# Kernel tuning notes

Hardware: AMD Instinct MI355X
Metric: run time of the kernel (lower is better)

## Reference

```python
import jax, jax.numpy as jnp
import numpy as np

N_GRAPHS = 100
BN_EPS = 1e-5
L = 4


def batch_norm(x, gamma, beta):
    # torch BatchNorm1d in training mode: biased batch statistics over the node dim
    mu = jnp.mean(x, axis=0)
    var = jnp.var(x, axis=0)
    return gamma * (x - mu) * jax.lax.rsqrt(var + BN_EPS) + beta


def setup_inputs() -> dict:
    key = jax.random.key(0)
    ks = jax.random.split(key, 24)
    N, E, IN, H, C = 50000, 600000, 128, 128, 10
    s = 0.05
    inp = {
        "h": jax.random.normal(ks[0], (N, IN), jnp.float32),
        "snorm_n": jax.random.uniform(ks[1], (N, 1), jnp.float32),
        "edge_src": jax.random.randint(ks[2], (E,), 0, N, jnp.int32),
        "edge_dst": jax.random.randint(ks[3], (E,), 0, N, jnp.int32),
        "graph_ids": jnp.sort(jax.random.randint(ks[4], (N,), 0, N_GRAPHS, jnp.int32)),
        # embedding_h
        "emb_W": jax.random.normal(ks[5], (IN, H), jnp.float32) * s,
        "emb_b": jnp.zeros((H,), jnp.float32),
        # per-layer GIN params, stacked over L layers
        "eps": jnp.zeros((L,), jnp.float32),
        "W1": jax.random.normal(ks[6], (L, H, H), jnp.float32) * s,
        "b1": jnp.zeros((L, H), jnp.float32),
        "g1": jnp.ones((L, H), jnp.float32),   # MLP internal BN gamma
        "be1": jnp.zeros((L, H), jnp.float32),  # MLP internal BN beta
        "W2": jax.random.normal(ks[7], (L, H, H), jnp.float32) * s,
        "b2": jnp.zeros((L, H), jnp.float32),
        "ga": jnp.ones((L, H), jnp.float32),    # ApplyNodeFunc BN gamma
        "ba": jnp.zeros((L, H), jnp.float32),
        "gl": jnp.ones((L, H), jnp.float32),    # GINLayer node BN gamma
        "bl": jnp.zeros((L, H), jnp.float32),
        # linears_prediction (L+1 of them)
        "pred_W": jax.random.normal(ks[8], (L + 1, H, C), jnp.float32) * s,
        "pred_b": jnp.zeros((L + 1, C), jnp.float32),
    }
    return inp


def reference(h, snorm_n, edge_src, edge_dst, graph_ids, emb_W, emb_b, eps,
              W1, b1, g1, be1, W2, b2, ga, ba, gl, bl, pred_W, pred_b):
    N = h.shape[0]
    h = h @ emb_W + emb_b  # embedding_h
    hidden_rep = [h]
    for i in range(L):
        h_in = h
        # sum-aggregate neighbor features (irregular gather + scatter-add)
        neigh = jax.ops.segment_sum(h[edge_src], edge_dst, num_segments=N)
        z = (1.0 + eps[i]) * h + neigh
        # ApplyNodeFunc: MLP (lin->BN->relu->lin) then BN then relu
        z = jax.nn.relu(batch_norm(z @ W1[i] + b1[i], g1[i], be1[i]))
        z = z @ W2[i] + b2[i]
        z = jax.nn.relu(batch_norm(z, ga[i], ba[i]))
        z = z * snorm_n                      # graph_norm
        z = batch_norm(z, gl[i], bl[i])      # batch_norm
        z = jax.nn.relu(z)
        h = h_in + z                         # residual (dropout p=0)
        hidden_rep.append(h)
    score = jnp.zeros((N_GRAPHS, pred_W.shape[-1]), h.dtype)
    for i, hr in enumerate(hidden_rep):
        pooled = jax.ops.segment_sum(hr, graph_ids, num_segments=N_GRAPHS)
        score = score + pooled @ pred_W[i] + pred_b[i]
    return score
```

## Files before the change

kernel.cpp:

```cpp
#include <hip/hip_runtime.h>

#define HD __device__ __forceinline__

static constexpr int H = 128;
static constexpr int G = 100;
static constexpr int L = 4;
static constexpr int C = 10;
static constexpr int DEGCAP = 64;

typedef __attribute__((ext_vector_type(8))) short short8;
typedef __attribute__((ext_vector_type(4))) float f32x4;

HD float bf2f(unsigned int u16) {
    return __uint_as_float(u16 << 16);
}
HD unsigned int f2bf(float f) {
    unsigned int u = __float_as_uint(f);
    u += 0x7fffu + ((u >> 16) & 1u);
    return u >> 16;
}

__global__ __launch_bounds__(256) void wprep_kernel(const float* __restrict__ embW,
                                                    const float* __restrict__ W1,
                                                    const float* __restrict__ W2,
                                                    unsigned short* __restrict__ WT) {
    int mat = blockIdx.y;
    const float* src = (mat == 0) ? embW
                     : (mat <= L) ? W1 + (size_t)(mat - 1) * H * H
                                  : W2 + (size_t)(mat - 1 - L) * H * H;
    int t = blockIdx.x * 256 + threadIdx.x;
    int col = t >> 7, k = t & 127;
    WT[(size_t)mat * H * H + col * H + k] = (unsigned short)f2bf(src[(size_t)k * H + col]);
}

__global__ void fill_kernel(const int* __restrict__ src, const int* __restrict__ dst, int E,
                            int* __restrict__ cnt, int* __restrict__ esrc) {
    int e = blockIdx.x * blockDim.x + threadIdx.x;
    if (e < E) {
        int d = dst[e];
        int pos = atomicAdd(&cnt[d], 1) & (DEGCAP - 1);
        esrc[(size_t)d * DEGCAP + pos] = src[e];
    }
}

__global__ __launch_bounds__(256, 4) void aggemm_kernel(
    const unsigned short* __restrict__ Hb, const int* __restrict__ cnt,
    const int* __restrict__ esrc, const float* __restrict__ eps, int layer,
    const unsigned short* __restrict__ WT, const float* __restrict__ bias,
    unsigned short* __restrict__ outB, int N,
    float* __restrict__ sum_out, float* __restrict__ sq_out) {
    __shared__ unsigned short As[64 * 136];
    int tid = threadIdx.x;
    int w = tid >> 6, lane = tid & 63, q = lane >> 4, m = lane & 15;
    int row0 = blockIdx.x * 64;
    int colbase = w * 32;

    short8 bfrag[2][4];
#pragma unroll
    for (int nt = 0; nt < 2; ++nt) {
        const unsigned short* wc = WT + (size_t)(colbase + nt * 16 + m) * H;
#pragma unroll
        for (int kk = 0; kk < 4; ++kk)
            bfrag[nt][kk] = *(const short8*)&wc[kk * 32 + q * 8];
    }

    const unsigned int* H2 = (const unsigned int*)Hb;
    float e1 = 1.0f + eps[layer];
    for (int i = 0; i < 16; ++i) {
        int r = w * 16 + i;
        int node = row0 + r;
        unsigned int out = 0;
        if (node < N) {
            unsigned int hv = H2[(size_t)node * 64 + lane];
            float ax[8], ay[8];
            ax[0] = e1 * bf2f(hv & 0xffffu);
            ay[0] = e1 * bf2f(hv >> 16);
#pragma unroll
            for (int u = 1; u < 8; ++u) { ax[u] = 0.f; ay[u] = 0.f; }
            int deg = min(cnt[node], DEGCAP);
            const int* ep = esrc + (size_t)node * DEGCAP;
            int j = 0;
            for (; j + 7 < deg; j += 8) {
                unsigned int v[8];
#pragma unroll
                for (int u = 0; u < 8; ++u) v[u] = H2[(size_t)ep[j + u] * 64 + lane];
#pragma unroll
                for (int u = 0; u < 8; ++u) {
                    ax[u] += bf2f(v[u] & 0xffffu);
                    ay[u] += bf2f(v[u] >> 16);
                }
            }
            for (; j + 1 < deg; j += 2) {
                unsigned int v0 = H2[(size_t)ep[j] * 64 + lane];
                unsigned int v1 = H2[(size_t)ep[j + 1] * 64 + lane];
                ax[0] += bf2f(v0 & 0xffffu); ay[0] += bf2f(v0 >> 16);
                ax[1] += bf2f(v1 & 0xffffu); ay[1] += bf2f(v1 >> 16);
            }
            if (j < deg) {
                unsigned int v0 = H2[(size_t)ep[j] * 64 + lane];
                ax[0] += bf2f(v0 & 0xffffu); ay[0] += bf2f(v0 >> 16);
            }
            float axs = ((ax[0] + ax[1]) + (ax[2] + ax[3])) + ((ax[4] + ax[5]) + (ax[6] + ax[7]));
            float ays = ((ay[0] + ay[1]) + (ay[2] + ay[3])) + ((ay[4] + ay[5]) + (ay[6] + ay[7]));
            out = f2bf(axs) | (f2bf(ays) << 16);
        }
        *(unsigned int*)&As[r * 136 + lane * 2] = out;
    }
    __syncthreads();

    f32x4 acc[4][2];
#pragma unroll
    for (int mt = 0; mt < 4; ++mt)
#pragma unroll
        for (int nt = 0; nt < 2; ++nt) acc[mt][nt] = (f32x4){0.f, 0.f, 0.f, 0.f};
#pragma unroll
    for (int kk = 0; kk < 4; ++kk) {
        short8 af[4];
#pragma unroll
        for (int mt = 0; mt < 4; ++mt)
            af[mt] = *(const short8*)&As[(mt * 16 + m) * 136 + kk * 32 + q * 8];
#pragma unroll
        for (int mt = 0; mt < 4; ++mt)
#pragma unroll
            for (int nt = 0; nt < 2; ++nt)
                acc[mt][nt] = __builtin_amdgcn_mfma_f32_16x16x32_bf16(
                    af[mt], bfrag[nt][kk], acc[mt][nt], 0, 0, 0);
    }

    float bs2[2] = {bias[colbase + m], bias[colbase + 16 + m]};
    float s[2] = {0.f, 0.f}, qq[2] = {0.f, 0.f};
#pragma unroll
    for (int mt = 0; mt < 4; ++mt)
#pragma unroll
        for (int nt = 0; nt < 2; ++nt) {
            int gcol = colbase + nt * 16 + m;
#pragma unroll
            for (int rg = 0; rg < 4; ++rg) {
                int grow = row0 + mt * 16 + q * 4 + rg;
                float v = acc[mt][nt][rg] + bs2[nt];
                if (grow < N) {
                    outB[(size_t)grow * H + gcol] = (unsigned short)f2bf(v);
                    s[nt] += v;
                    qq[nt] += v * v;
                }
            }
        }
#pragma unroll
    for (int nt = 0; nt < 2; ++nt) {
        float sv = s[nt], qv = qq[nt];
        sv += __shfl_xor(sv, 16); sv += __shfl_xor(sv, 32);
        qv += __shfl_xor(qv, 16); qv += __shfl_xor(qv, 32);
        if (q == 0) {
            atomicAdd(&sum_out[colbase + nt * 16 + m], sv);
            atomicAdd(&sq_out[colbase + nt * 16 + m], qv);
        }
    }
}

template <bool ABF16, bool TRANS, bool STATS, bool POOLF>
__global__ __launch_bounds__(256, 4) void mgemm_kernel(
    const float* __restrict__ Af, const unsigned short* __restrict__ Ab,
    const unsigned short* __restrict__ WT, const float* __restrict__ bias,
    const float* __restrict__ sum_in, const float* __restrict__ sq_in,
    const float* __restrict__ gam, const float* __restrict__ bet, float invN,
    unsigned short* __restrict__ outB,
    int N, float* __restrict__ sum_out, float* __restrict__ sq_out,
    const int* __restrict__ gids, float* __restrict__ pool) {
    __shared__ unsigned short As[64 * 136];
    __shared__ float cas[H], ccs[H];
    int tid = threadIdx.x;
    int w = tid >> 6, lane = tid & 63, q = lane >> 4, m = lane & 15;
    int row0 = blockIdx.x * 64;
    int colbase = w * 32;

    short8 bfrag[2][4];
#pragma unroll
    for (int nt = 0; nt < 2; ++nt) {
        const unsigned short* wc = WT + (size_t)(colbase + nt * 16 + m) * H;
#pragma unroll
        for (int kk = 0; kk < 4; ++kk)
            bfrag[nt][kk] = *(const short8*)&wc[kk * 32 + q * 8];
    }

    if (TRANS) {
        if (tid < H) {
            float mu = sum_in[tid] * invN;
            float var = sq_in[tid] * invN - mu * mu;
            float inv = rsqrtf(var + 1e-5f);
            float a = gam[tid] * inv;
            cas[tid] = a;
            ccs[tid] = bet[tid] - mu * a;
        }
        __syncthreads();
    }

    {
        int cc = tid & 15, rg = tid >> 4;
        int c0 = cc * 8;
        float a8[8], b8[8];
        if (TRANS) {
#pragma unroll
            for (int j = 0; j < 8; ++j) { a8[j] = cas[c0 + j]; b8[j] = ccs[c0 + j]; }
        }
#pragma unroll
        for (int rr = 0; rr < 4; ++rr) {
            int r = rg * 4 + rr;
            int gr = row0 + r;
            uint4 o = {0u, 0u, 0u, 0u};
            if (ABF16 && !TRANS) {
                if (gr < N) o = *(const uint4*)&Ab[(size_t)gr * H + c0];
            } else {
                float v[8] = {0.f, 0.f, 0.f, 0.f, 0.f, 0.f, 0.f, 0.f};
                if (gr < N) {
                    if (ABF16) {
                        uint4 x = *(const uint4*)&Ab[(size_t)gr * H + c0];
                        v[0] = bf2f(x.x & 0xffffu); v[1] = bf2f(x.x >> 16);
                        v[2] = bf2f(x.y & 0xffffu); v[3] = bf2f(x.y >> 16);
                        v[4] = bf2f(x.z & 0xffffu); v[5] = bf2f(x.z >> 16);
                        v[6] = bf2f(x.w & 0xffffu); v[7] = bf2f(x.w >> 16);
                    } else {
                        float4 x0 = *(const float4*)&Af[(size_t)gr * H + c0];
                        float4 x1 = *(const float4*)&Af[(size_t)gr * H + c0 + 4];
                        v[0] = x0.x; v[1] = x0.y; v[2] = x0.z; v[3] = x0.w;
                        v[4] = x1.x; v[5] = x1.y; v[6] = x1.z; v[7] = x1.w;
                    }
                }
                if (TRANS) {
#pragma unroll
                    for (int j = 0; j < 8; ++j) v[j] = fmaxf(a8[j] * v[j] + b8[j], 0.f);
                }
                o.x = f2bf(v[0]) | (f2bf(v[1]) << 16);
                o.y = f2bf(v[2]) | (f2bf(v[3]) << 16);
                o.z = f2bf(v[4]) | (f2bf(v[5]) << 16);
                o.w = f2bf(v[6]) | (f2bf(v[7]) << 16);
            }
            *(uint4*)&As[r * 136 + c0] = o;
        }
    }
    __syncthreads();

    f32x4 acc[4][2];
#pragma unroll
    for (int mt = 0; mt < 4; ++mt)
#pragma unroll
        for (int nt = 0; nt < 2; ++nt) acc[mt][nt] = (f32x4){0.f, 0.f, 0.f, 0.f};
#pragma unroll
    for (int kk = 0; kk < 4; ++kk) {
        short8 af[4];
#pragma unroll
        for (int mt = 0; mt < 4; ++mt)
            af[mt] = *(const short8*)&As[(mt * 16 + m) * 136 + kk * 32 + q * 8];
#pragma unroll
        for (int mt = 0; mt < 4; ++mt)
#pragma unroll
            for (int nt = 0; nt < 2; ++nt)
                acc[mt][nt] = __builtin_amdgcn_mfma_f32_16x16x32_bf16(
                    af[mt], bfrag[nt][kk], acc[mt][nt], 0, 0, 0);
    }

    float bs2[2] = {bias[colbase + m], bias[colbase + 16 + m]};
    float s[2] = {0.f, 0.f}, qq[2] = {0.f, 0.f};
#pragma unroll
    for (int mt = 0; mt < 4; ++mt)
#pragma unroll
        for (int nt = 0; nt < 2; ++nt) {
            int gcol = colbase + nt * 16 + m;
#pragma unroll
            for (int rg = 0; rg < 4; ++rg) {
                int grow = row0 + mt * 16 + q * 4 + rg;
                float v = acc[mt][nt][rg] + bs2[nt];
                if (grow < N) {
                    outB[(size_t)grow * H + gcol] = (unsigned short)f2bf(v);
                    if (STATS || POOLF) {
                        s[nt] += v;
                        if (STATS) qq[nt] += v * v;
                    }
                }
            }
        }

    if (STATS) {
#pragma unroll
        for (int nt = 0; nt < 2; ++nt) {
            float sv = s[nt], qv = qq[nt];
            sv += __shfl_xor(sv, 16); sv += __shfl_xor(sv, 32);
            qv += __shfl_xor(qv, 16); qv += __shfl_xor(qv, 32);
            if (q == 0) {
                atomicAdd(&sum_out[colbase + nt * 16 + m], sv);
                atomicAdd(&sq_out[colbase + nt * 16 + m], qv);
            }
        }
    }

    if (POOLF) {
        int last = min(row0 + 63, N - 1);
        bool uni = (gids[row0] == gids[last]);
        if (uni) {
            int g = gids[row0];
#pragma unroll
            for (int nt = 0; nt < 2; ++nt) {
                float sv = s[nt];
                sv += __shfl_xor(sv, 16); sv += __shfl_xor(sv, 32);
                if (q == 0) atomicAdd(&pool[g * H + colbase + nt * 16 + m], sv);
            }
        } else {
#pragma unroll
            for (int mt = 0; mt < 4; ++mt)
#pragma unroll
                for (int nt = 0; nt < 2; ++nt)
#pragma unroll
                    for (int rg = 0; rg < 4; ++rg) {
                        int grow = row0 + mt * 16 + q * 4 + rg;
                        if (grow < N) {
                            float v = acc[mt][nt][rg] + bs2[nt];
                            atomicAdd(&pool[gids[grow] * H + colbase + nt * 16 + m], v);
                        }
                    }
        }
    }
}

__global__ __launch_bounds__(256) void statsv_kernel(const unsigned short* __restrict__ UB,
                                                     const float* __restrict__ snorm,
                                                     const float* __restrict__ sum2, const float* __restrict__ sq2,
                                                     const float* __restrict__ ga, const float* __restrict__ ba,
                                                     float invN, int N,
                                                     float* __restrict__ sum3, float* __restrict__ sq3) {
    __shared__ float cas[H], ccs[H];
    int t = threadIdx.x;
    if (t < H) {
        float m = sum2[t] * invN;
        float var = sq2[t] * invN - m * m;
        float inv = rsqrtf(var + 1e-5f);
        float a = ga[t] * inv;
        cas[t] = a;
        ccs[t] = ba[t] - m * a;
    }
    __syncthreads();
    int col2 = t & 63, part = t >> 6;
    int c0 = col2 * 2, c1 = c0 + 1;
    float a0 = cas[c0], b0 = ccs[c0], a1 = cas[c1], b1 = ccs[c1];
    float s0 = 0.f, q0 = 0.f, s1 = 0.f, q1 = 0.f;
    const unsigned int* U2 = (const unsigned int*)UB;
    for (int r = blockIdx.x * 4 + part; r < N; r += gridDim.x * 4) {
        float sn = snorm[r];
        unsigned int v = U2[(size_t)r * 64 + col2];
        float v0 = fmaxf(a0 * bf2f(v & 0xffffu) + b0, 0.f) * sn;
        float v1 = fmaxf(a1 * bf2f(v >> 16) + b1, 0.f) * sn;
        s0 += v0; q0 += v0 * v0;
        s1 += v1; q1 += v1 * v1;
    }
    __shared__ float S[4][H], Q[4][H];
    S[part][c0] = s0; S[part][c1] = s1;
    Q[part][c0] = q0; Q[part][c1] = q1;
    __syncthreads();
    if (t < H) {
        atomicAdd(&sum3[t], S[0][t] + S[1][t] + S[2][t] + S[3][t]);
        atomicAdd(&sq3[t], Q[0][t] + Q[1][t] + Q[2][t] + Q[3][t]);
    }
}

__global__ __launch_bounds__(256) void tail_kernel(unsigned short* __restrict__ Hb,
                                                   const unsigned short* __restrict__ UB,
                                                   const float* __restrict__ snorm,
                                                   const float* __restrict__ sum2, const float* __restrict__ sq2,
                                                   const float* __restrict__ ga, const float* __restrict__ ba,
                                                   const float* __restrict__ sum3, const float* __restrict__ sq3,
                                                   const float* __restrict__ gl, const float* __restrict__ bl,
                                                   float invN, const int* __restrict__ gids,
                                                   float* __restrict__ pool, int N) {
    __shared__ float ca2[H], cc2[H], ca3[H], cc3[H];
    __shared__ float PS[8][H];
    int t = threadIdx.x;
    if (t < H) {
        float m2 = sum2[t] * invN, v2 = sq2[t] * invN - m2 * m2;
        float i2 = rsqrtf(v2 + 1e-5f), a2 = ga[t] * i2;
        ca2[t] = a2; cc2[t] = ba[t] - m2 * a2;
        float m3 = sum3[t] * invN, v3 = sq3[t] * invN - m3 * m3;
        float i3 = rsqrtf(v3 + 1e-5f), a3 = gl[t] * i3;
        ca3[t] = a3; cc3[t] = bl[t] - m3 * a3;
    }
    __syncthreads();
    int row0 = blockIdx.x * 32;
    int col4 = t & 31, rowg = t >> 5;
    int c0 = col4 * 4;
    float A2[4], B2[4], A3[4], B3[4];
#pragma unroll
    for (int j = 0; j < 4; ++j) {
        A2[j] = ca2[c0 + j]; B2[j] = cc2[c0 + j];
        A3[j] = ca3[c0 + j]; B3[j] = cc3[c0 + j];
    }
    bool uni = (gids[row0] == gids[min(row0 + 31, N - 1)]);
    float p[4] = {0.f, 0.f, 0.f, 0.f};
    const uint2* U4 = (const uint2*)UB;
    uint2* H4 = (uint2*)Hb;
#pragma unroll
    for (int rr = 0; rr < 4; ++rr) {
        int r = row0 + rowg * 4 + rr;
        if (r < N) {
            float sn = snorm[r];
            uint2 uv = U4[(size_t)r * 32 + col4];
            uint2 hv = H4[(size_t)r * 32 + col4];
            float u[4] = {bf2f(uv.x & 0xffffu), bf2f(uv.x >> 16), bf2f(uv.y & 0xffffu), bf2f(uv.y >> 16)};
            float h[4] = {bf2f(hv.x & 0xffffu), bf2f(hv.x >> 16), bf2f(hv.y & 0xffffu), bf2f(hv.y >> 16)};
#pragma unroll
            for (int j = 0; j < 4; ++j) {
                float v = fmaxf(A2[j] * u[j] + B2[j], 0.f) * sn;
                h[j] += fmaxf(A3[j] * v + B3[j], 0.f);
            }
            uint2 hb;
            hb.x = f2bf(h[0]) | (f2bf(h[1]) << 16);
            hb.y = f2bf(h[2]) | (f2bf(h[3]) << 16);
            H4[(size_t)r * 32 + col4] = hb;
            if (uni) {
                p[0] += h[0]; p[1] += h[1]; p[2] += h[2]; p[3] += h[3];
            } else {
                int g = gids[r];
#pragma unroll
                for (int j = 0; j < 4; ++j) atomicAdd(&pool[g * H + c0 + j], h[j]);
            }
        }
    }
    if (uni) {
#pragma unroll
        for (int j = 0; j < 4; ++j) PS[rowg][c0 + j] = p[j];
        __syncthreads();
        if (t < H) {
            float s = PS[0][t] + PS[1][t] + PS[2][t] + PS[3][t] +
                      PS[4][t] + PS[5][t] + PS[6][t] + PS[7][t];
            atomicAdd(&pool[gids[row0] * H + t], s);
        }
    }
}

__global__ void final_kernel(const float* __restrict__ pool, const float* __restrict__ pw,
                             const float* __restrict__ pb, float* __restrict__ out) {
    int g = blockIdx.x, t = threadIdx.x;
    __shared__ float p[H];
    float acc = 0.f;
    for (int i = 0; i <= L; ++i) {
        p[t] = pool[(size_t)(i * G + g) * H + t];
        __syncthreads();
        if (t < C) {
            float s = 0.f;
            for (int f = 0; f < H; ++f) s += p[f] * pw[(size_t)(i * H + f) * C + t];
            acc += s + pb[i * C + t];
        }
        __syncthreads();
    }
    if (t < C) out[g * C + t] = acc;
}

extern "C" void kernel_launch(void* const* d_in, const int* in_sizes, int n_in,
                              void* d_out, int out_size, void* d_ws, size_t ws_size,
                              hipStream_t stream) {
    const float* h_in  = (const float*)d_in[0];
    const float* snorm = (const float*)d_in[1];
    const int* esrc_in = (const int*)d_in[2];
    const int* edst_in = (const int*)d_in[3];
    const int* gids    = (const int*)d_in[4];
    const float* embW = (const float*)d_in[5];
    const float* embB = (const float*)d_in[6];
    const float* eps  = (const float*)d_in[7];
    const float* W1   = (const float*)d_in[8];
    const float* b1   = (const float*)d_in[9];
    const float* g1   = (const float*)d_in[10];
    const float* be1  = (const float*)d_in[11];
    const float* W2   = (const float*)d_in[12];
    const float* b2   = (const float*)d_in[13];
    const float* ga   = (const float*)d_in[14];
    const float* ba   = (const float*)d_in[15];
    const float* gl   = (const float*)d_in[16];
    const float* bl   = (const float*)d_in[17];
    const float* predW = (const float*)d_in[18];
    const float* predB = (const float*)d_in[19];

    const int N = in_sizes[0] / H;
    const int E = in_sizes[2];
    const float invN = 1.0f / (float)N;

    float* ws = (float*)d_ws;
    float* POOL = ws;
    float* STATS = POOL + (size_t)(L + 1) * G * H;
    int* CNT = (int*)(STATS + (size_t)L * 6 * H);
    unsigned short* WT = (unsigned short*)(CNT + N);
    int* ESRC = (int*)(WT + (size_t)9 * H * H);
    unsigned short* Hb = (unsigned short*)(ESRC + (size_t)N * DEGCAP);
    unsigned short* TB = Hb + (size_t)N * H;
    unsigned short* UB = TB + (size_t)N * H;

    size_t zbytes = ((size_t)(L + 1) * G * H + (size_t)L * 6 * H + N) * 4;
    hipMemsetAsync(POOL, 0, zbytes, stream);

    wprep_kernel<<<dim3(64, 9), 256, 0, stream>>>(embW, W1, W2, WT);
    fill_kernel<<<(E + 255) / 256, 256, 0, stream>>>(esrc_in, edst_in, E, CNT, ESRC);

    int gblocks = (N + 63) / 64;
    mgemm_kernel<false, false, false, true><<<gblocks, 256, 0, stream>>>(
        h_in, nullptr, WT, embB, nullptr, nullptr, nullptr, nullptr, invN,
        Hb, N, nullptr, nullptr, gids, POOL);

    for (int i = 0; i < L; ++i) {
        float* S1 = STATS + (size_t)i * 6 * H;
        float* Q1 = S1 + H;
        float* S2 = Q1 + H;
        float* Q2 = S2 + H;
        float* S3 = Q2 + H;
        float* Q3 = S3 + H;
        aggemm_kernel<<<gblocks, 256, 0, stream>>>(
            Hb, CNT, ESRC, eps, i, WT + (size_t)(1 + i) * H * H, b1 + (size_t)i * H,
            TB, N, S1, Q1);
        mgemm_kernel<true, true, true, false><<<gblocks, 256, 0, stream>>>(
            nullptr, TB, WT + (size_t)(1 + L + i) * H * H, b2 + (size_t)i * H,
            S1, Q1, g1 + (size_t)i * H, be1 + (size_t)i * H, invN,
            UB, N, S2, Q2, nullptr, nullptr);
        statsv_kernel<<<256, 256, 0, stream>>>(UB, snorm, S2, Q2,
                                               ga + (size_t)i * H, ba + (size_t)i * H, invN, N, S3, Q3);
        tail_kernel<<<(N + 31) / 32, 256, 0, stream>>>(Hb, UB, snorm,
                                                       S2, Q2, ga + (size_t)i * H, ba + (size_t)i * H,
                                                       S3, Q3, gl + (size_t)i * H, bl + (size_t)i * H,
                                                       invN, gids, POOL + (size_t)(i + 1) * G * H, N);
    }
    final_kernel<<<G, H, 0, stream>>>(POOL, predW, predB, (float*)d_out);
}
```

Measured before the change: 741.3 us.

## Fuse all GIN layers into one cooperative persistent kernel with grid syncs

```diff
diff --git a/kernel.cpp b/kernel.cpp
--- a/kernel.cpp
+++ b/kernel.cpp
@@ -1,4 +1,7 @@
 #include <hip/hip_runtime.h>
+#include <hip/hip_cooperative_groups.h>
+
+namespace cg = cooperative_groups;
 
 #define HD __device__ __forceinline__
 
@@ -43,12 +46,22 @@
     }
 }
 
-__global__ __launch_bounds__(256, 4) void aggemm_kernel(
-    const unsigned short* __restrict__ Hb, const int* __restrict__ cnt,
-    const int* __restrict__ esrc, const float* __restrict__ eps, int layer,
-    const unsigned short* __restrict__ WT, const float* __restrict__ bias,
-    unsigned short* __restrict__ outB, int N,
-    float* __restrict__ sum_out, float* __restrict__ sq_out) {
+__global__ void pad_kernel(const int* __restrict__ cnt, int* __restrict__ esrc,
+                           unsigned short* __restrict__ Hb, int N) {
+    int n = blockIdx.x * 256 + threadIdx.x;
+    if (n < N) {
+        int deg = min(cnt[n], DEGCAP);
+        int degPad = min((deg + 15) & ~15, DEGCAP);
+        for (int k = deg; k < degPad; ++k) esrc[(size_t)n * DEGCAP + k] = N;
+    }
+    if (blockIdx.x == 0 && threadIdx.x < 64)
+        ((unsigned int*)(Hb + (size_t)N * H))[threadIdx.x] = 0u;
+}
+
+__global__ __launch_bounds__(256, 4) void egemm_kernel(
+    const float* __restrict__ Af, const unsigned short* __restrict__ WT,
+    const float* __restrict__ bias, unsigned short* __restrict__ outB, int N,
+    const int* __restrict__ gids, float* __restrict__ pool) {
     __shared__ unsigned short As[64 * 136];
     int tid = threadIdx.x;
     int w = tid >> 6, lane = tid & 63, q = lane >> 4, m = lane & 15;
@@ -64,47 +77,24 @@
             bfrag[nt][kk] = *(const short8*)&wc[kk * 32 + q * 8];
     }
 
-    const unsigned int* H2 = (const unsigned int*)Hb;
-    float e1 = 1.0f + eps[layer];
-    for (int i = 0; i < 16; ++i) {
-        int r = w * 16 + i;
-        int node = row0 + r;
-        unsigned int out = 0;
-        if (node < N) {
-            unsigned int hv = H2[(size_t)node * 64 + lane];
-            float ax[8], ay[8];
-            ax[0] = e1 * bf2f(hv & 0xffffu);
-            ay[0] = e1 * bf2f(hv >> 16);
-#pragma unroll
-            for (int u = 1; u < 8; ++u) { ax[u] = 0.f; ay[u] = 0.f; }
-            int deg = min(cnt[node], DEGCAP);
-            const int* ep = esrc + (size_t)node * DEGCAP;
-            int j = 0;
-            for (; j + 7 < deg; j += 8) {
-                unsigned int v[8];
-#pragma unroll
-                for (int u = 0; u < 8; ++u) v[u] = H2[(size_t)ep[j + u] * 64 + lane];
-#pragma unroll
-                for (int u = 0; u < 8; ++u) {
-                    ax[u] += bf2f(v[u] & 0xffffu);
-                    ay[u] += bf2f(v[u] >> 16);
-                }
-            }
-            for (; j + 1 < deg; j += 2) {
-                unsigned int v0 = H2[(size_t)ep[j] * 64 + lane];
-                unsigned int v1 = H2[(size_t)ep[j + 1] * 64 + lane];
-                ax[0] += bf2f(v0 & 0xffffu); ay[0] += bf2f(v0 >> 16);
-                ax[1] += bf2f(v1 & 0xffffu); ay[1] += bf2f(v1 >> 16);
-            }
-            if (j < deg) {
-                unsigned int v0 = H2[(size_t)ep[j] * 64 + lane];
-                ax[0] += bf2f(v0 & 0xffffu); ay[0] += bf2f(v0 >> 16);
-            }
-            float axs = ((ax[0] + ax[1]) + (ax[2] + ax[3])) + ((ax[4] + ax[5]) + (ax[6] + ax[7]));
-            float ays = ((ay[0] + ay[1]) + (ay[2] + ay[3])) + ((ay[4] + ay[5]) + (ay[6] + ay[7]));
-            out = f2bf(axs) | (f2bf(ays) << 16);
-        }
-        *(unsigned int*)&As[r * 136 + lane * 2] = out;
+    {
+        int cc = tid & 15, rg = tid >> 4;
+        int c0 = cc * 8;
+#pragma unroll
+        for (int rr = 0; rr < 4; ++rr) {
+            int r = rg * 4 + rr;
+            int gr = row0 + r;
+            uint4 o = {0u, 0u, 0u, 0u};
+            if (gr < N) {
+                float4 x0 = *(const float4*)&Af[(size_t)gr * H + c0];
+                float4 x1 = *(const float4*)&Af[(size_t)gr * H + c0 + 4];
+                o.x = f2bf(x0.x) | (f2bf(x0.y) << 16);
+                o.y = f2bf(x0.z) | (f2bf(x0.w) << 16);
+                o.z = f2bf(x1.x) | (f2bf(x1.y) << 16);
+                o.w = f2bf(x1.z) | (f2bf(x1.w) << 16);
+            }
+            *(uint4*)&As[r * 136 + c0] = o;
+        }
     }
     __syncthreads();
 
@@ -128,7 +118,7 @@
     }
 
     float bs2[2] = {bias[colbase + m], bias[colbase + 16 + m]};
-    float s[2] = {0.f, 0.f}, qq[2] = {0.f, 0.f};
+    float s[2] = {0.f, 0.f};
 #pragma unroll
     for (int mt = 0; mt < 4; ++mt)
 #pragma unroll
@@ -141,47 +131,56 @@
                 if (grow < N) {
                     outB[(size_t)grow * H + gcol] = (unsigned short)f2bf(v);
                     s[nt] += v;
-                    qq[nt] += v * v;
-                }
-            }
-        }
-#pragma unroll
-    for (int nt = 0; nt < 2; ++nt) {
-        float sv = s[nt], qv = qq[nt];
-        sv += __shfl_xor(sv, 16); sv += __shfl_xor(sv, 32);
-        qv += __shfl_xor(qv, 16); qv += __shfl_xor(qv, 32);
-        if (q == 0) {
-            atomicAdd(&sum_out[colbase + nt * 16 + m], sv);
-            atomicAdd(&sq_out[colbase + nt * 16 + m], qv);
-        }
-    }
-}
-
-template <bool ABF16, bool TRANS, bool STATS, bool POOLF>
-__global__ __launch_bounds__(256, 4) void mgemm_kernel(
-    const float* __restrict__ Af, const unsigned short* __restrict__ Ab,
-    const unsigned short* __restrict__ WT, const float* __restrict__ bias,
-    const float* __restrict__ sum_in, const float* __restrict__ sq_in,
-    const float* __restrict__ gam, const float* __restrict__ bet, float invN,
-    unsigned short* __restrict__ outB,
-    int N, float* __restrict__ sum_out, float* __restrict__ sq_out,
-    const int* __restrict__ gids, float* __restrict__ pool) {
-    __shared__ unsigned short As[64 * 136];
-    __shared__ float cas[H], ccs[H];
+                }
+            }
+        }
+
+    int last = min(row0 + 63, N - 1);
+    bool uni = (gids[row0] == gids[last]);
+    if (uni) {
+        int g = gids[row0];
+#pragma unroll
+        for (int nt = 0; nt < 2; ++nt) {
+            float sv = s[nt];
+            sv += __shfl_xor(sv, 16); sv += __shfl_xor(sv, 32);
+            if (q == 0) atomicAdd(&pool[g * H + colbase + nt * 16 + m], sv);
+        }
+    } else {
+#pragma unroll
+        for (int mt = 0; mt < 4; ++mt)
+#pragma unroll
+            for (int nt = 0; nt < 2; ++nt)
+#pragma unroll
+                for (int rg = 0; rg < 4; ++rg) {
+                    int grow = row0 + mt * 16 + q * 4 + rg;
+                    if (grow < N) {
+                        float v = acc[mt][nt][rg] + bs2[nt];
+                        atomicAdd(&pool[gids[grow] * H + colbase + nt * 16 + m], v);
+                    }
+                }
+    }
+}
+
+template <bool TRANS>
+HD void gemm_phase(unsigned short* As, float* cas, float* ccs,
+                   const unsigned short* __restrict__ Ab, const unsigned short* __restrict__ WTl,
+                   const float* __restrict__ bias,
+                   const float* __restrict__ sum_in, const float* __restrict__ sq_in,
+                   const float* __restrict__ gam, const float* __restrict__ bet,
+                   float invN, unsigned short* __restrict__ outB, int N, int tiles,
+                   float* __restrict__ sum_out, float* __restrict__ sq_out) {
     int tid = threadIdx.x;
     int w = tid >> 6, lane = tid & 63, q = lane >> 4, m = lane & 15;
-    int row0 = blockIdx.x * 64;
     int colbase = w * 32;
 
     short8 bfrag[2][4];
 #pragma unroll
     for (int nt = 0; nt < 2; ++nt) {
-        const unsigned short* wc = WT + (size_t)(colbase + nt * 16 + m) * H;
+        const unsigned short* wc = WTl + (size_t)(colbase + nt * 16 + m) * H;
 #pragma unroll
         for (int kk = 0; kk < 4; ++kk)
             bfrag[nt][kk] = *(const short8*)&wc[kk * 32 + q * 8];
     }
-
     if (TRANS) {
         if (tid < H) {
             float mu = sum_in[tid] * invN;
@@ -191,95 +190,82 @@
             cas[tid] = a;
             ccs[tid] = bet[tid] - mu * a;
         }
-        __syncthreads();
-    }
-
-    {
-        int cc = tid & 15, rg = tid >> 4;
-        int c0 = cc * 8;
-        float a8[8], b8[8];
-        if (TRANS) {
-#pragma unroll
-            for (int j = 0; j < 8; ++j) { a8[j] = cas[c0 + j]; b8[j] = ccs[c0 + j]; }
-        }
+    }
+    __syncthreads();
+
+    int cc = tid & 15, rg = tid >> 4;
+    int c0 = cc * 8;
+    float a8[8], b8[8];
+    if (TRANS) {
+#pragma unroll
+        for (int j = 0; j < 8; ++j) { a8[j] = cas[c0 + j]; b8[j] = ccs[c0 + j]; }
+    }
+    float bs2[2] = {bias[colbase + m], bias[colbase + 16 + m]};
+
+    for (int t = blockIdx.x; t < tiles; t += gridDim.x) {
+        int row0 = t * 64;
 #pragma unroll
         for (int rr = 0; rr < 4; ++rr) {
             int r = rg * 4 + rr;
             int gr = row0 + r;
             uint4 o = {0u, 0u, 0u, 0u};
-            if (ABF16 && !TRANS) {
+            if (!TRANS) {
                 if (gr < N) o = *(const uint4*)&Ab[(size_t)gr * H + c0];
             } else {
-                float v[8] = {0.f, 0.f, 0.f, 0.f, 0.f, 0.f, 0.f, 0.f};
                 if (gr < N) {
-                    if (ABF16) {
-                        uint4 x = *(const uint4*)&Ab[(size_t)gr * H + c0];
-                        v[0] = bf2f(x.x & 0xffffu); v[1] = bf2f(x.x >> 16);
-                        v[2] = bf2f(x.y & 0xffffu); v[3] = bf2f(x.y >> 16);
-                        v[4] = bf2f(x.z & 0xffffu); v[5] = bf2f(x.z >> 16);
-                        v[6] = bf2f(x.w & 0xffffu); v[7] = bf2f(x.w >> 16);
-                    } else {
-                        float4 x0 = *(const float4*)&Af[(size_t)gr * H + c0];
-                        float4 x1 = *(const float4*)&Af[(size_t)gr * H + c0 + 4];
-                        v[0] = x0.x; v[1] = x0.y; v[2] = x0.z; v[3] = x0.w;
-                        v[4] = x1.x; v[5] = x1.y; v[6] = x1.z; v[7] = x1.w;
+                    uint4 x = *(const uint4*)&Ab[(size_t)gr * H + c0];
+                    float v[8] = {bf2f(x.x & 0xffffu), bf2f(x.x >> 16),
+                                  bf2f(x.y & 0xffffu), bf2f(x.y >> 16),
+                                  bf2f(x.z & 0xffffu), bf2f(x.z >> 16),
+                                  bf2f(x.w & 0xffffu), bf2f(x.w >> 16)};
+#pragma unroll
+                    for (int j = 0; j < 8; ++j) v[j] = fmaxf(a8[j] * v[j] + b8[j], 0.f);
+                    o.x = f2bf(v[0]) | (f2bf(v[1]) << 16);
+                    o.y = f2bf(v[2]) | (f2bf(v[3]) << 16);
+                    o.z = f2bf(v[4]) | (f2bf(v[5]) << 16);
+                    o.w = f2bf(v[6]) | (f2bf(v[7]) << 16);
+                }
+            }
+            *(uint4*)&As[r * 136 + c0] = o;
+        }
+        __syncthreads();
+
+        f32x4 acc[4][2];
+#pragma unroll
+        for (int mt = 0; mt < 4; ++mt)
+#pragma unroll
+            for (int nt = 0; nt < 2; ++nt) acc[mt][nt] = (f32x4){0.f, 0.f, 0.f, 0.f};
+#pragma unroll
+        for (int kk = 0; kk < 4; ++kk) {
+            short8 af[4];
+#pragma unroll
+            for (int mt = 0; mt < 4; ++mt)
+                af[mt] = *(const short8*)&As[(mt * 16 + m) * 136 + kk * 32 + q * 8];
+#pragma unroll
+            for (int mt = 0; mt < 4; ++mt)
+#pragma unroll
+                for (int nt = 0; nt < 2; ++nt)
+                    acc[mt][nt] = __builtin_amdgcn_mfma_f32_16x16x32_bf16(
+                        af[mt], bfrag[nt][kk], acc[mt][nt], 0, 0, 0);
+        }
+
+        float s[2] = {0.f, 0.f}, qq[2] = {0.f, 0.f};
+#pragma unroll
+        for (int mt = 0; mt < 4; ++mt)
+#pragma unroll
+            for (int nt = 0; nt < 2; ++nt) {
+                int gcol = colbase + nt * 16 + m;
+#pragma unroll
+                for (int rg2 = 0; rg2 < 4; ++rg2) {
+                    int grow = row0 + mt * 16 + q * 4 + rg2;
+                    float v = acc[mt][nt][rg2] + bs2[nt];
+                    if (grow < N) {
+                        outB[(size_t)grow * H + gcol] = (unsigned short)f2bf(v);
+                        s[nt] += v;
+                        qq[nt] += v * v;
                     }
                 }
-                if (TRANS) {
-#pragma unroll
-                    for (int j = 0; j < 8; ++j) v[j] = fmaxf(a8[j] * v[j] + b8[j], 0.f);
-                }
-                o.x = f2bf(v[0]) | (f2bf(v[1]) << 16);
-                o.y = f2bf(v[2]) | (f2bf(v[3]) << 16);
-                o.z = f2bf(v[4]) | (f2bf(v[5]) << 16);
-                o.w = f2bf(v[6]) | (f2bf(v[7]) << 16);
-            }
-            *(uint4*)&As[r * 136 + c0] = o;
-        }
-    }
-    __syncthreads();
-
-    f32x4 acc[4][2];
-#pragma unroll
-    for (int mt = 0; mt < 4; ++mt)
-#pragma unroll
-        for (int nt = 0; nt < 2; ++nt) acc[mt][nt] = (f32x4){0.f, 0.f, 0.f, 0.f};
-#pragma unroll
-    for (int kk = 0; kk < 4; ++kk) {
-        short8 af[4];
-#pragma unroll
-        for (int mt = 0; mt < 4; ++mt)
-            af[mt] = *(const short8*)&As[(mt * 16 + m) * 136 + kk * 32 + q * 8];
-#pragma unroll
-        for (int mt = 0; mt < 4; ++mt)
-#pragma unroll
-            for (int nt = 0; nt < 2; ++nt)
-                acc[mt][nt] = __builtin_amdgcn_mfma_f32_16x16x32_bf16(
-                    af[mt], bfrag[nt][kk], acc[mt][nt], 0, 0, 0);
-    }
-
-    float bs2[2] = {bias[colbase + m], bias[colbase + 16 + m]};
-    float s[2] = {0.f, 0.f}, qq[2] = {0.f, 0.f};
-#pragma unroll
-    for (int mt = 0; mt < 4; ++mt)
-#pragma unroll
-        for (int nt = 0; nt < 2; ++nt) {
-            int gcol = colbase + nt * 16 + m;
-#pragma unroll
-            for (int rg = 0; rg < 4; ++rg) {
-                int grow = row0 + mt * 16 + q * 4 + rg;
-                float v = acc[mt][nt][rg] + bs2[nt];
-                if (grow < N) {
-                    outB[(size_t)grow * H + gcol] = (unsigned short)f2bf(v);
-                    if (STATS || POOLF) {
-                        s[nt] += v;
-                        if (STATS) qq[nt] += v * v;
-                    }
-                }
-            }
-        }
-
-    if (STATS) {
+            }
 #pragma unroll
         for (int nt = 0; nt < 2; ++nt) {
             float sv = s[nt], qv = qq[nt];
@@ -290,146 +276,188 @@
                 atomicAdd(&sq_out[colbase + nt * 16 + m], qv);
             }
         }
-    }
-
-    if (POOLF) {
-        int last = min(row0 + 63, N - 1);
-        bool uni = (gids[row0] == gids[last]);
-        if (uni) {
-            int g = gids[row0];
-#pragma unroll
-            for (int nt = 0; nt < 2; ++nt) {
-                float sv = s[nt];
-                sv += __shfl_xor(sv, 16); sv += __shfl_xor(sv, 32);
-                if (q == 0) atomicAdd(&pool[g * H + colbase + nt * 16 + m], sv);
-            }
-        } else {
-#pragma unroll
-            for (int mt = 0; mt < 4; ++mt)
-#pragma unroll
-                for (int nt = 0; nt < 2; ++nt)
-#pragma unroll
-                    for (int rg = 0; rg < 4; ++rg) {
-                        int grow = row0 + mt * 16 + q * 4 + rg;
-                        if (grow < N) {
-                            float v = acc[mt][nt][rg] + bs2[nt];
-                            atomicAdd(&pool[gids[grow] * H + colbase + nt * 16 + m], v);
+        __syncthreads();
+    }
+}
+
+__global__ __launch_bounds__(256, 4) void mega_kernel(
+    const unsigned short* __restrict__ WT,
+    unsigned short* __restrict__ Hb, unsigned short* __restrict__ ZB,
+    unsigned short* __restrict__ TB, unsigned short* __restrict__ UB,
+    const int* __restrict__ cnt, const int* __restrict__ esrc,
+    const float* __restrict__ eps,
+    const float* __restrict__ b1, const float* __restrict__ g1, const float* __restrict__ be1,
+    const float* __restrict__ b2, const float* __restrict__ ga, const float* __restrict__ ba,
+    const float* __restrict__ gl, const float* __restrict__ bl,
+    const float* __restrict__ snorm, const int* __restrict__ gids,
+    float* __restrict__ POOL, float* __restrict__ STATS, int N, float invN) {
+    cg::grid_group grid = cg::this_grid();
+    __shared__ __align__(16) unsigned char smem[19456];
+    unsigned short* As = (unsigned short*)smem;
+    float* c1 = (float*)(smem + 17408);
+    float* c2 = c1 + H;
+    float* c3 = c2 + H;
+    float* c4 = c3 + H;
+
+    int tid = threadIdx.x;
+    int w = tid >> 6, lane = tid & 63;
+    int tiles64 = (N + 63) / 64;
+    int tiles32 = (N + 31) / 32;
+    const unsigned int* H2 = (const unsigned int*)Hb;
+
+    for (int layer = 0; layer < L; ++layer) {
+        float* S1 = STATS + (size_t)layer * 6 * H;
+        float* Q1 = S1 + H;
+        float* S2 = Q1 + H;
+        float* Q2 = S2 + H;
+        float* S3 = Q2 + H;
+        float* Q3 = S3 + H;
+        const unsigned short* W1l = WT + (size_t)(1 + layer) * H * H;
+        const unsigned short* W2l = WT + (size_t)(1 + L + layer) * H * H;
+
+        {
+            float e1 = 1.0f + eps[layer];
+            int wid = blockIdx.x * 4 + w;
+            int stride = gridDim.x * 4;
+            for (int node = wid; node < N; node += stride) {
+                unsigned int hv = H2[(size_t)node * 64 + lane];
+                int deg = min(cnt[node], DEGCAP);
+                int degPad = min((deg + 15) & ~15, DEGCAP);
+                const int* ep = esrc + (size_t)node * DEGCAP;
+                float ax = e1 * bf2f(hv & 0xffffu);
+                float ay = e1 * bf2f(hv >> 16);
+                for (int j = 0; j < degPad; j += 16) {
+                    unsigned int v[16];
+#pragma unroll
+                    for (int u = 0; u < 16; ++u) v[u] = H2[(size_t)ep[j + u] * 64 + lane];
+                    float sx[4] = {0.f, 0.f, 0.f, 0.f}, sy[4] = {0.f, 0.f, 0.f, 0.f};
+#pragma unroll
+                    for (int u = 0; u < 16; ++u) {
+                        sx[u & 3] += bf2f(v[u] & 0xffffu);
+                        sy[u & 3] += bf2f(v[u] >> 16);
+                    }
+                    ax += (sx[0] + sx[1]) + (sx[2] + sx[3]);
+                    ay += (sy[0] + sy[1]) + (sy[2] + sy[3]);
+                }
+                ((unsigned int*)ZB)[(size_t)node * 64 + lane] = f2bf(ax) | (f2bf(ay) << 16);
+            }
+        }
+        grid.sync();
+
+        gemm_phase<false>(As, c1, c2, ZB, W1l, b1 + (size_t)layer * H,
+                          nullptr, nullptr, nullptr, nullptr, invN, TB, N, tiles64, S1, Q1);
+        grid.sync();
+
+        gemm_phase<true>(As, c1, c2, TB, W2l, b2 + (size_t)layer * H,
+                         S1, Q1, g1 + (size_t)layer * H, be1 + (size_t)layer * H,
+                         invN, UB, N, tiles64, S2, Q2);
+        grid.sync();
+
+        {
+            if (tid < H) {
+                float mu = S2[tid] * invN;
+                float var = Q2[tid] * invN - mu * mu;
+                float inv = rsqrtf(var + 1e-5f);
+                float a = ga[(size_t)layer * H + tid] * inv;
+                c1[tid] = a;
+                c2[tid] = ba[(size_t)layer * H + tid] - mu * a;
+            }
+            __syncthreads();
+            int col2 = tid & 63, part = tid >> 6;
+            int cA = col2 * 2, cB = cA + 1;
+            float a0 = c1[cA], b0 = c2[cA], a1 = c1[cB], b1c = c2[cB];
+            float s0 = 0.f, q0 = 0.f, s1 = 0.f, q1 = 0.f;
+            const unsigned int* U2 = (const unsigned int*)UB;
+            for (int r = blockIdx.x * 4 + part; r < N; r += gridDim.x * 4) {
+                float sn = snorm[r];
+                unsigned int v = U2[(size_t)r * 64 + col2];
+                float v0 = fmaxf(a0 * bf2f(v & 0xffffu) + b0, 0.f) * sn;
+                float v1 = fmaxf(a1 * bf2f(v >> 16) + b1c, 0.f) * sn;
+                s0 += v0; q0 += v0 * v0;
+                s1 += v1; q1 += v1 * v1;
+            }
+            float* SSm = (float*)As;
+            float* QQm = SSm + 4 * H;
+            SSm[part * H + cA] = s0; SSm[part * H + cB] = s1;
+            QQm[part * H + cA] = q0; QQm[part * H + cB] = q1;
+            __syncthreads();
+            if (tid < H) {
+                atomicAdd(&S3[tid], SSm[tid] + SSm[H + tid] + SSm[2 * H + tid] + SSm[3 * H + tid]);
+                atomicAdd(&Q3[tid], QQm[tid] + QQm[H + tid] + QQm[2 * H + tid] + QQm[3 * H + tid]);
+            }
+            __syncthreads();
+        }
+        grid.sync();
+
+        {
+            if (tid < H) {
+                float m2 = S2[tid] * invN, v2 = Q2[tid] * invN - m2 * m2;
+                float i2 = rsqrtf(v2 + 1e-5f), a2 = ga[(size_t)layer * H + tid] * i2;
+                c1[tid] = a2; c2[tid] = ba[(size_t)layer * H + tid] - m2 * a2;
+                float m3 = S3[tid] * invN, v3 = Q3[tid] * invN - m3 * m3;
+                float i3 = rsqrtf(v3 + 1e-5f), a3 = gl[(size_t)layer * H + tid] * i3;
+                c3[tid] = a3; c4[tid] = bl[(size_t)layer * H + tid] - m3 * a3;
+            }
+            __syncthreads();
+            float* PS = (float*)As;
+            float* poolL = POOL + (size_t)(layer + 1) * G * H;
+            int col4 = tid & 31, rowg = tid >> 5;
+            int c0 = col4 * 4;
+            float A2[4], B2[4], A3[4], B3[4];
+#pragma unroll
+            for (int j = 0; j < 4; ++j) {
+                A2[j] = c1[c0 + j]; B2[j] = c2[c0 + j];
+                A3[j] = c3[c0 + j]; B3[j] = c4[c0 + j];
+            }
+            const uint2* U4 = (const uint2*)UB;
+            uint2* H4 = (uint2*)Hb;
+            for (int t32 = blockIdx.x; t32 < tiles32; t32 += gridDim.x) {
+                int row0 = t32 * 32;
+                bool uni = (gids[row0] == gids[min(row0 + 31, N - 1)]);
+                float p[4] = {0.f, 0.f, 0.f, 0.f};
+#pragma unroll
+                for (int rr = 0; rr < 4; ++rr) {
+                    int r = row0 + rowg * 4 + rr;
+                    if (r < N) {
+                        float sn = snorm[r];
+                        uint2 uv = U4[(size_t)r * 32 + col4];
+                        uint2 hv = H4[(size_t)r * 32 + col4];
+                        float u[4] = {bf2f(uv.x & 0xffffu), bf2f(uv.x >> 16),
+                                      bf2f(uv.y & 0xffffu), bf2f(uv.y >> 16)};
+                        float h[4] = {bf2f(hv.x & 0xffffu), bf2f(hv.x >> 16),
+                                      bf2f(hv.y & 0xffffu), bf2f(hv.y >> 16)};
+#pragma unroll
+                        for (int j = 0; j < 4; ++j) {
+                            float v = fmaxf(A2[j] * u[j] + B2[j], 0.f) * sn;
+                            h[j] += fmaxf(A3[j] * v + B3[j], 0.f);
+                        }
+                        uint2 hb;
+                        hb.x = f2bf(h[0]) | (f2bf(h[1]) << 16);
+                        hb.y = f2bf(h[2]) | (f2bf(h[3]) << 16);
+                        H4[(size_t)r * 32 + col4] = hb;
+                        if (uni) {
+                            p[0] += h[0]; p[1] += h[1]; p[2] += h[2]; p[3] += h[3];
+                        } else {
+                            int g = gids[r];
+#pragma unroll
+                            for (int j = 0; j < 4; ++j) atomicAdd(&poolL[g * H + c0 + j], h[j]);
                         }
                     }
-        }
-    }
-}
-
-__global__ __launch_bounds__(256) void statsv_kernel(const unsigned short* __restrict__ UB,
-                                                     const float* __restrict__ snorm,
-                                                     const float* __restrict__ sum2, const float* __restrict__ sq2,
-                                                     const float* __restrict__ ga, const float* __restrict__ ba,
-                                                     float invN, int N,
-                                                     float* __restrict__ sum3, float* __restrict__ sq3) {
-    __shared__ float cas[H], ccs[H];
-    int t = threadIdx.x;
-    if (t < H) {
-        float m = sum2[t] * invN;
-        float var = sq2[t] * invN - m * m;
-        float inv = rsqrtf(var + 1e-5f);
-        float a = ga[t] * inv;
-        cas[t] = a;
-        ccs[t] = ba[t] - m * a;
-    }
-    __syncthreads();
-    int col2 = t & 63, part = t >> 6;
-    int c0 = col2 * 2, c1 = c0 + 1;
-    float a0 = cas[c0], b0 = ccs[c0], a1 = cas[c1], b1 = ccs[c1];
-    float s0 = 0.f, q0 = 0.f, s1 = 0.f, q1 = 0.f;
-    const unsigned int* U2 = (const unsigned int*)UB;
-    for (int r = blockIdx.x * 4 + part; r < N; r += gridDim.x * 4) {
-        float sn = snorm[r];
-        unsigned int v = U2[(size_t)r * 64 + col2];
-        float v0 = fmaxf(a0 * bf2f(v & 0xffffu) + b0, 0.f) * sn;
-        float v1 = fmaxf(a1 * bf2f(v >> 16) + b1, 0.f) * sn;
-        s0 += v0; q0 += v0 * v0;
-        s1 += v1; q1 += v1 * v1;
-    }
-    __shared__ float S[4][H], Q[4][H];
-    S[part][c0] = s0; S[part][c1] = s1;
-    Q[part][c0] = q0; Q[part][c1] = q1;
-    __syncthreads();
-    if (t < H) {
-        atomicAdd(&sum3[t], S[0][t] + S[1][t] + S[2][t] + S[3][t]);
-        atomicAdd(&sq3[t], Q[0][t] + Q[1][t] + Q[2][t] + Q[3][t]);
-    }
-}
-
-__global__ __launch_bounds__(256) void tail_kernel(unsigned short* __restrict__ Hb,
-                                                   const unsigned short* __restrict__ UB,
-                                                   const float* __restrict__ snorm,
-                                                   const float* __restrict__ sum2, const float* __restrict__ sq2,
-                                                   const float* __restrict__ ga, const float* __restrict__ ba,
-                                                   const float* __restrict__ sum3, const float* __restrict__ sq3,
-                                                   const float* __restrict__ gl, const float* __restrict__ bl,
-                                                   float invN, const int* __restrict__ gids,
-                                                   float* __restrict__ pool, int N) {
-    __shared__ float ca2[H], cc2[H], ca3[H], cc3[H];
-    __shared__ float PS[8][H];
-    int t = threadIdx.x;
-    if (t < H) {
-        float m2 = sum2[t] * invN, v2 = sq2[t] * invN - m2 * m2;
-        float i2 = rsqrtf(v2 + 1e-5f), a2 = ga[t] * i2;
-        ca2[t] = a2; cc2[t] = ba[t] - m2 * a2;
-        float m3 = sum3[t] * invN, v3 = sq3[t] * invN - m3 * m3;
-        float i3 = rsqrtf(v3 + 1e-5f), a3 = gl[t] * i3;
-        ca3[t] = a3; cc3[t] = bl[t] - m3 * a3;
-    }
-    __syncthreads();
-    int row0 = blockIdx.x * 32;
-    int col4 = t & 31, rowg = t >> 5;
-    int c0 = col4 * 4;
-    float A2[4], B2[4], A3[4], B3[4];
-#pragma unroll
-    for (int j = 0; j < 4; ++j) {
-        A2[j] = ca2[c0 + j]; B2[j] = cc2[c0 + j];
-        A3[j] = ca3[c0 + j]; B3[j] = cc3[c0 + j];
-    }
-    bool uni = (gids[row0] == gids[min(row0 + 31, N - 1)]);
-    float p[4] = {0.f, 0.f, 0.f, 0.f};
-    const uint2* U4 = (const uint2*)UB;
-    uint2* H4 = (uint2*)Hb;
-#pragma unroll
-    for (int rr = 0; rr < 4; ++rr) {
-        int r = row0 + rowg * 4 + rr;
-        if (r < N) {
-            float sn = snorm[r];
-            uint2 uv = U4[(size_t)r * 32 + col4];
-            uint2 hv = H4[(size_t)r * 32 + col4];
-            float u[4] = {bf2f(uv.x & 0xffffu), bf2f(uv.x >> 16), bf2f(uv.y & 0xffffu), bf2f(uv.y >> 16)};
-            float h[4] = {bf2f(hv.x & 0xffffu), bf2f(hv.x >> 16), bf2f(hv.y & 0xffffu), bf2f(hv.y >> 16)};
-#pragma unroll
-            for (int j = 0; j < 4; ++j) {
-                float v = fmaxf(A2[j] * u[j] + B2[j], 0.f) * sn;
-                h[j] += fmaxf(A3[j] * v + B3[j], 0.f);
-            }
-            uint2 hb;
-            hb.x = f2bf(h[0]) | (f2bf(h[1]) << 16);
-            hb.y = f2bf(h[2]) | (f2bf(h[3]) << 16);
-            H4[(size_t)r * 32 + col4] = hb;
-            if (uni) {
-                p[0] += h[0]; p[1] += h[1]; p[2] += h[2]; p[3] += h[3];
-            } else {
-                int g = gids[r];
-#pragma unroll
-                for (int j = 0; j < 4; ++j) atomicAdd(&pool[g * H + c0 + j], h[j]);
-            }
-        }
-    }
-    if (uni) {
-#pragma unroll
-        for (int j = 0; j < 4; ++j) PS[rowg][c0 + j] = p[j];
-        __syncthreads();
-        if (t < H) {
-            float s = PS[0][t] + PS[1][t] + PS[2][t] + PS[3][t] +
-                      PS[4][t] + PS[5][t] + PS[6][t] + PS[7][t];
-            atomicAdd(&pool[gids[row0] * H + t], s);
-        }
+                }
+                if (uni) {
+#pragma unroll
+                    for (int j = 0; j < 4; ++j) PS[rowg * H + c0 + j] = p[j];
+                    __syncthreads();
+                    if (tid < H) {
+                        float s = PS[tid] + PS[H + tid] + PS[2 * H + tid] + PS[3 * H + tid] +
+                                  PS[4 * H + tid] + PS[5 * H + tid] + PS[6 * H + tid] + PS[7 * H + tid];
+                        atomicAdd(&poolL[gids[row0] * H + tid], s);
+                    }
+                    __syncthreads();
+                }
+            }
+        }
+        grid.sync();
     }
 }
 
@@ -486,40 +514,39 @@
     unsigned short* WT = (unsigned short*)(CNT + N);
     int* ESRC = (int*)(WT + (size_t)9 * H * H);
     unsigned short* Hb = (unsigned short*)(ESRC + (size_t)N * DEGCAP);
-    unsigned short* TB = Hb + (size_t)N * H;
-    unsigned short* UB = TB + (size_t)N * H;
+    unsigned short* ZB = Hb + (size_t)(N + 1) * H;
+    unsigned short* TB = ZB + (size_t)N * H;
+    unsigned short* UB = ZB;
 
     size_t zbytes = ((size_t)(L + 1) * G * H + (size_t)L * 6 * H + N) * 4;
     hipMemsetAsync(POOL, 0, zbytes, stream);
 
     wprep_kernel<<<dim3(64, 9), 256, 0, stream>>>(embW, W1, W2, WT);
     fill_kernel<<<(E + 255) / 256, 256, 0, stream>>>(esrc_in, edst_in, E, CNT, ESRC);
+    pad_kernel<<<(N + 255) / 256, 256, 0, stream>>>(CNT, ESRC, Hb, N);
 
     int gblocks = (N + 63) / 64;
-    mgemm_kernel<false, false, false, true><<<gblocks, 256, 0, stream>>>(
-        h_in, nullptr, WT, embB, nullptr, nullptr, nullptr, nullptr, invN,
-        Hb, N, nullptr, nullptr, gids, POOL);
-
-    for (int i = 0; i < L; ++i) {
-        float* S1 = STATS + (size_t)i * 6 * H;
-        float* Q1 = S1 + H;
-        float* S2 = Q1 + H;
-        float* Q2 = S2 + H;
-        float* S3 = Q2 + H;
-        float* Q3 = S3 + H;
-        aggemm_kernel<<<gblocks, 256, 0, stream>>>(
-            Hb, CNT, ESRC, eps, i, WT + (size_t)(1 + i) * H * H, b1 + (size_t)i * H,
-            TB, N, S1, Q1);
-        mgemm_kernel<true, true, true, false><<<gblocks, 256, 0, stream>>>(
-            nullptr, TB, WT + (size_t)(1 + L + i) * H * H, b2 + (size_t)i * H,
-            S1, Q1, g1 + (size_t)i * H, be1 + (size_t)i * H, invN,
-            UB, N, S2, Q2, nullptr, nullptr);
-        statsv_kernel<<<256, 256, 0, stream>>>(UB, snorm, S2, Q2,
-                                               ga + (size_t)i * H, ba + (size_t)i * H, invN, N, S3, Q3);
-        tail_kernel<<<(N + 31) / 32, 256, 0, stream>>>(Hb, UB, snorm,
-                                                       S2, Q2, ga + (size_t)i * H, ba + (size_t)i * H,
-                                                       S3, Q3, gl + (size_t)i * H, bl + (size_t)i * H,
-                                                       invN, gids, POOL + (size_t)(i + 1) * G * H, N);
-    }
+    egemm_kernel<<<gblocks, 256, 0, stream>>>(h_in, WT, embB, Hb, N, gids, POOL);
+
+    int occ = 0;
+    hipOccupancyMaxActiveBlocksPerMultiprocessor(&occ, mega_kernel, 256, 0);
+    if (occ < 1) occ = 1;
+    if (occ > 4) occ = 4;
+    dim3 mgrid(256 * occ);
+    unsigned short* Hb_a = Hb;  unsigned short* ZB_a = ZB;
+    unsigned short* TB_a = TB;  unsigned short* UB_a = UB;
+    const unsigned short* WT_a = WT;
+    const int* CNT_a = CNT;  const int* ESRC_a = ESRC;
+    float* POOL_a = POOL;  float* STATS_a = STATS;
+    int N_a = N;  float invN_a = invN;
+    void* args[] = {
+        (void*)&WT_a, (void*)&Hb_a, (void*)&ZB_a, (void*)&TB_a, (void*)&UB_a,
+        (void*)&CNT_a, (void*)&ESRC_a, (void*)&eps,
+        (void*)&b1, (void*)&g1, (void*)&be1, (void*)&b2,
+        (void*)&ga, (void*)&ba, (void*)&gl, (void*)&bl,
+        (void*)&snorm, (void*)&gids, (void*)&POOL_a, (void*)&STATS_a,
+        (void*)&N_a, (void*)&invN_a};
+    hipLaunchCooperativeKernel((const void*)mega_kernel, mgrid, dim3(256), args, 0, stream);
+
     final_kernel<<<G, H, 0, stream>>>(POOL, predW, predB, (float*)d_out);
 }
```

Measured after the change: 1.781 ms. +140.2%, slower.
